# Kernel tuning notes

Hardware: AMD Instinct MI355X
Metric: run time of the kernel (lower is better)

## Reference

```python
import jax, jax.numpy as jnp
import numpy as np

HOP = jnp.array([0, 1, 4, 7, 2, 5, 8, 3, 6, 9, 11, 14, 10, 12, 15, 13, 16])
GRAPH = jnp.array([0, 1, 4, 7, 2, 5, 8, 3, 6, 9, 12, 10, 13, 15, 11, 14, 16])
D_MODEL, L, D_INNER, D_STATE, DT_RANK = 512, 17, 1024, 4, 32


def layernorm(x, w, b, eps=1e-5):
    mu = x.mean(-1, keepdims=True)
    var = ((x - mu) ** 2).mean(-1, keepdims=True)
    return (x - mu) * jax.lax.rsqrt(var + eps) * w + b


def setup_inputs() -> dict:
    key = jax.random.key(0)
    ks = jax.random.split(key, 9)
    B = 4096
    s = lambda k, shape: jax.random.normal(k, shape, jnp.float32) * 0.02
    # A_log init per mamba_ssm: log(1..d_state) repeated over d_inner
    A_log = jnp.log(jnp.broadcast_to(jnp.arange(1, D_STATE + 1, dtype=jnp.float32), (D_INNER, D_STATE)))
    return {
        "x": jax.random.normal(ks[0], (B, L, D_MODEL), jnp.float32),
        "bp_embed": s(ks[1], (1, 5, D_MODEL)),
        "ln_w": jnp.ones((D_MODEL,), jnp.float32),
        "ln_b": jnp.zeros((D_MODEL,), jnp.float32),
        "in_proj_w": s(ks[2], (2 * D_INNER, D_MODEL)),
        "conv_w": 1.0 + s(ks[3], (D_INNER,)),  # d_conv=1 depthwise conv == per-channel scale
        "conv_b": jnp.zeros((D_INNER,), jnp.float32),
        "x_proj_w": s(ks[4], (DT_RANK + 2 * D_STATE, D_INNER)),
        "dt_proj_w": s(ks[5], (D_INNER, DT_RANK)),
        "dt_proj_b": s(ks[6], (D_INNER,)) - 4.0,  # softplus-inverse-ish small dt init
        "A_log": A_log,
        "D": jnp.ones((D_INNER,), jnp.float32),
        "out_proj_w": s(ks[7], (D_MODEL, D_INNER)),
    }


def mamba(u, in_proj_w, conv_w, conv_b, x_proj_w, dt_proj_w, dt_proj_b, A_log, D, out_proj_w):
    # u: [B, L, d_model]
    xz = jnp.einsum('bld,ed->ble', u, in_proj_w)          # [B,L,2*d_inner]
    xm, z = jnp.split(xz, 2, axis=-1)
    xm = jax.nn.silu(xm * conv_w + conv_b)                 # d_conv=1 -> pointwise
    x_dbl = jnp.einsum('ble,fe->blf', xm, x_proj_w)        # [B,L,dt_rank+2*d_state]
    dt_r = x_dbl[..., :DT_RANK]
    Bm = x_dbl[..., DT_RANK:DT_RANK + D_STATE]
    Cm = x_dbl[..., DT_RANK + D_STATE:]
    dt = jax.nn.softplus(jnp.einsum('blr,er->ble', dt_r, dt_proj_w) + dt_proj_b)  # [B,L,d_inner]
    A = -jnp.exp(A_log)                                    # [d_inner,d_state]

    def step(h, inp):
        dt_t, B_t, C_t, x_t = inp                          # [B,di],[B,ds],[B,ds],[B,di]
        dA = jnp.exp(dt_t[..., None] * A)                  # [B,di,ds]
        h = dA * h + (dt_t * x_t)[..., None] * B_t[:, None, :]
        y = jnp.einsum('bes,bs->be', h, C_t)
        return h, y

    bsz = u.shape[0]
    h0 = jnp.zeros((bsz, D_INNER, D_STATE), u.dtype)
    seq = (dt.transpose(1, 0, 2), Bm.transpose(1, 0, 2), Cm.transpose(1, 0, 2), xm.transpose(1, 0, 2))
    _, ys = jax.lax.scan(step, h0, seq)                    # ys: [L,B,d_inner]
    y = ys.transpose(1, 0, 2) + xm * D
    y = y * jax.nn.silu(z)
    return jnp.einsum('ble,de->bld', y, out_proj_w)


def reference(x, bp_embed, ln_w, ln_b, in_proj_w, conv_w, conv_b, x_proj_w,
              dt_proj_w, dt_proj_b, A_log, D, out_proj_w):
    bp = bp_embed
    x_bpe = jnp.concatenate([bp[:, :3], bp[:, :3], bp[:, :3], bp[:, :1],
                             bp[:, 3:], bp[:, :1], bp[:, 3:], bp[:, 3:]], axis=1)  # [1,17,dim]
    x_ssm = x[:, HOP, :] + x_bpe
    x_ssm = layernorm(x_ssm, ln_w, ln_b)
    x_ssm = mamba(x_ssm, in_proj_w, conv_w, conv_b, x_proj_w,
                  dt_proj_w, dt_proj_b, A_log, D, out_proj_w)
    return x + x_ssm[:, GRAPH, :]
```

## Files before the change

### kernel.cpp

```cpp
#include <hip/hip_runtime.h>

typedef unsigned short u16;
typedef unsigned int   u32;
typedef __bf16 bf16_t;
typedef bf16_t bf16x8 __attribute__((ext_vector_type(8)));
typedef float  f32x4  __attribute__((ext_vector_type(4)));

#define DEV static __device__ __forceinline__

__constant__ int c_HOP[17] = {0,1,4,7,2,5,8,3,6,9,11,14,10,12,15,13,16};
__constant__ int c_BPE[17] = {0,1,2,0,1,2,0,1,2,0,3,4,0,3,4,3,4};

DEV u16 f2bf(float f){
  u32 x = __builtin_bit_cast(u32, f);
  x += 0x7fffu + ((x >> 16) & 1u);
  return (u16)(x >> 16);
}
DEV float bf2f(u32 u){ return __builtin_bit_cast(float, u << 16); }
DEV float silu_f(float v){ return v / (1.f + __expf(-v)); }
DEV float softplus_f(float s){ return (s > 20.f) ? s : log1pf(__expf(s)); }

DEV void gll16(const void* g, void* l){
  __builtin_amdgcn_global_load_lds((__attribute__((address_space(1))) void*)g,
                                   (__attribute__((address_space(3))) void*)l,
                                   16, 0, 0);
}

__global__ __launch_bounds__(256) void cvt4(
    const float* __restrict__ s0, u16* __restrict__ d0, int n0,
    const float* __restrict__ s1, u16* __restrict__ d1, int n1,
    const float* __restrict__ s2, u16* __restrict__ d2, int n2,
    const float* __restrict__ s3, u16* __restrict__ d3, int n3)
{
  int t = blockIdx.x * 256 + threadIdx.x;
  if (t < n0){ d0[t] = f2bf(s0[t]); return; }
  t -= n0; if (t < n1){ d1[t] = f2bf(s1[t]); return; }
  t -= n1; if (t < n2){ d2[t] = f2bf(s2[t]); return; }
  t -= n2; if (t < n3){ d3[t] = f2bf(s3[t]); }
}

__global__ __launch_bounds__(256) void ln_gather(
    const float* __restrict__ x, const float* __restrict__ bpe,
    const float* __restrict__ lnw, const float* __restrict__ lnb,
    u16* __restrict__ u)
{
  int tok = blockIdx.x;
  int b = tok / 17;
  int l = tok - b * 17;
  const float* xr = x   + ((size_t)b * 17 + c_HOP[l]) * 512;
  const float* br = bpe + (size_t)c_BPE[l] * 512;
  int tid = threadIdx.x;
  int d0 = tid * 2;
  float2 xv = *(const float2*)(xr + d0);
  float2 bv = *(const float2*)(br + d0);
  float v0 = xv.x + bv.x, v1 = xv.y + bv.y;

  __shared__ float red[8];
  float s = v0 + v1;
  #pragma unroll
  for (int o = 32; o; o >>= 1) s += __shfl_xor(s, o);
  if ((tid & 63) == 0) red[tid >> 6] = s;
  __syncthreads();
  float mu = (red[0] + red[1] + red[2] + red[3]) * (1.f / 512.f);
  float a0 = v0 - mu, a1 = v1 - mu;
  float q = a0 * a0 + a1 * a1;
  #pragma unroll
  for (int o = 32; o; o >>= 1) q += __shfl_xor(q, o);
  if ((tid & 63) == 0) red[4 + (tid >> 6)] = q;
  __syncthreads();
  float var = (red[4] + red[5] + red[6] + red[7]) * (1.f / 512.f);
  float rs = rsqrtf(var + 1e-5f);

  u16 o0 = f2bf(a0 * rs * lnw[d0]     + lnb[d0]);
  u16 o1 = f2bf(a1 * rs * lnw[d0 + 1] + lnb[d0 + 1]);
  u32 pack = (u32)o0 | ((u32)o1 << 16);
  *(u32*)(u + (size_t)tok * 512 + d0) = pack;
}

enum { EPI_SPLIT = 0, EPI_XDBL = 1, EPI_DT = 2, EPI_OUT = 3 };

template<int EPI>
__global__ __launch_bounds__(256) void gemm_bt(
    const u16* __restrict__ A, int lda,
    const u16* __restrict__ W, int K, int MT,
    u16* __restrict__ ob0, u16* __restrict__ ob1,
    const float* __restrict__ p0, const float* __restrict__ p1,
    const float* __restrict__ xres, float* __restrict__ fout)
{
  __shared__ u16 sA[2][128 * 32];
  __shared__ u16 sW[2][128 * 32];
  int nwg = gridDim.x;
  int cpx = nwg >> 3;
  int wg = (blockIdx.x & 7) * cpx + (blockIdx.x >> 3);
  int NT = nwg / MT;
  int nt = wg % NT, mt = wg / NT;
  int brow = mt * 128, bcol = nt * 128;
  int tid = threadIdx.x, lane = tid & 63, wid = tid >> 6;
  int wm = wid >> 1, wn = wid & 1;

  f32x4 acc[4][4] = {};

  int srow = tid >> 2;
  int sch  = tid & 3;

  const u16* gA0 = A + (size_t)(brow + srow)      * lda + (sch ^ ((srow >> 1) & 3)) * 8;
  const u16* gA1 = A + (size_t)(brow + 64 + srow) * lda + (sch ^ (((64 + srow) >> 1) & 3)) * 8;
  const u16* gW0 = W + (size_t)(bcol + srow)      * K   + (sch ^ ((srow >> 1) & 3)) * 8;
  const u16* gW1 = W + (size_t)(bcol + 64 + srow) * K   + (sch ^ (((64 + srow) >> 1) & 3)) * 8;

  auto STAGE = [&](int buf, int kt) {
    gll16(gA0 + kt, (char*)sA[buf] + tid * 16);
    gll16(gA1 + kt, (char*)sA[buf] + tid * 16 + 4096);
    gll16(gW0 + kt, (char*)sW[buf] + tid * 16);
    gll16(gW1 + kt, (char*)sW[buf] + tid * 16 + 4096);
  };

  int aoff[4], boff[4];
  #pragma unroll
  for (int mi = 0; mi < 4; mi++) {
    int r = wm * 64 + mi * 16 + (lane & 15);
    int c = (lane >> 4) ^ ((r >> 1) & 3);
    aoff[mi] = r * 64 + c * 16;
  }
  #pragma unroll
  for (int ni = 0; ni < 4; ni++) {
    int r = wn * 64 + ni * 16 + (lane & 15);
    int c = (lane >> 4) ^ ((r >> 1) & 3);
    boff[ni] = r * 64 + c * 16;
  }

  auto COMPUTE = [&](int buf) {
    bf16x8 av[4], bv[4];
    #pragma unroll
    for (int mi = 0; mi < 4; mi++)
      av[mi] = *(const bf16x8*)((const char*)sA[buf] + aoff[mi]);
    #pragma unroll
    for (int ni = 0; ni < 4; ni++)
      bv[ni] = *(const bf16x8*)((const char*)sW[buf] + boff[ni]);
    #pragma unroll
    for (int mi = 0; mi < 4; mi++)
      #pragma unroll
      for (int ni = 0; ni < 4; ni++)
        acc[mi][ni] = __builtin_amdgcn_mfma_f32_16x16x32_bf16(
            av[mi], bv[ni], acc[mi][ni], 0, 0, 0);
  };

  int nsteps = K >> 5;
  STAGE(0, 0);
  __syncthreads();
  for (int s = 0; s < nsteps; s += 2) {
    if (s + 1 < nsteps) STAGE(1, (s + 1) << 5);
    COMPUTE(0);
    __syncthreads();
    if (s + 1 < nsteps) {
      if (s + 2 < nsteps) STAGE(0, (s + 2) << 5);
      COMPUTE(1);
      __syncthreads();
    }
  }

  int r4 = (lane >> 4) * 4;
  int cl = lane & 15;
  #pragma unroll
  for (int mi = 0; mi < 4; mi++) {
    int rowb = brow + wm * 64 + mi * 16 + r4;
    #pragma unroll
    for (int ni = 0; ni < 4; ni++) {
      int col = bcol + wn * 64 + ni * 16 + cl;
      if constexpr (EPI == EPI_SPLIT) {
        bool isx = (col < 1024);
        float cw = isx ? p0[col] : 1.f;
        float cb = isx ? p1[col] : 0.f;
        u16* dst = isx ? (ob0 + col) : (ob1 + col - 1024);
        #pragma unroll
        for (int rr = 0; rr < 4; rr++)
          dst[(size_t)(rowb + rr) * 1024] = f2bf(silu_f(acc[mi][ni][rr] * cw + cb));
      } else if constexpr (EPI == EPI_XDBL) {
        if (col < 40) {
          #pragma unroll
          for (int rr = 0; rr < 4; rr++)
            ob0[(size_t)(rowb + rr) * 40 + col] = f2bf(acc[mi][ni][rr]);
        }
      } else if constexpr (EPI == EPI_DT) {
        float bb = p0[col];
        #pragma unroll
        for (int rr = 0; rr < 4; rr++)
          ob0[(size_t)(rowb + rr) * 1024 + col] = f2bf(softplus_f(acc[mi][ni][rr] + bb));
      } else {
        #pragma unroll
        for (int rr = 0; rr < 4; rr++) {
          int row = rowb + rr;
          u32 rw = (u32)row;
          u32 b = rw / 17u;
          int gl = (int)(rw - b * 17u);
          size_t oi = ((size_t)b * 17 + c_HOP[gl]) * 512 + col;
          fout[oi] = xres[oi] + acc[mi][ni][rr];
        }
      }
    }
  }
}

__global__ __launch_bounds__(128) void scan5(
    const u16* __restrict__ xm, const u16* __restrict__ zs,
    const u16* __restrict__ xdbl, u16* __restrict__ dty,
    const float* __restrict__ A_log, const float* __restrict__ Dp)
{
  int b = blockIdx.x;
  int tid = threadIdx.x;
  int e0 = tid * 8;
  const size_t base = (size_t)b * 17 * 1024;

  float4 al = *(const float4*)(A_log + (size_t)e0 * 4);
  float A0 = -__expf(al.x), A1 = -__expf(al.y);
  float A2 = -__expf(al.z), A3 = -__expf(al.w);
  float Dv[8];
  *(float4*)(Dv)     = *(const float4*)(Dp + e0);
  *(float4*)(Dv + 4) = *(const float4*)(Dp + e0 + 4);

  const u16* xmb = xm + base + e0;
  const u16* zsb = zs + base + e0;
  u16* db = dty + base + e0;
  const u16* bcb = xdbl + (size_t)b * 680 + 32;

  float h[8][4];
  #pragma unroll
  for (int c = 0; c < 8; c++)
    #pragma unroll
    for (int s = 0; s < 4; s++) h[c][s] = 0.f;

  #pragma unroll
  for (int t = 0; t < 17; t++) {
    uint4 xr = *(const uint4*)(xmb + t * 1024);
    uint4 zr = *(const uint4*)(zsb + t * 1024);
    uint4 dr = *(const uint4*)(db + t * 1024);
    uint4 bc = *(const uint4*)(bcb + t * 40);
    float B0 = bf2f(bc.x & 0xffffu), B1 = bf2f(bc.x >> 16);
    float B2 = bf2f(bc.y & 0xffffu), B3 = bf2f(bc.y >> 16);
    float C0 = bf2f(bc.z & 0xffffu), C1 = bf2f(bc.z >> 16);
    float C2 = bf2f(bc.w & 0xffffu), C3 = bf2f(bc.w >> 16);
    u32 yo[4];
    const u32* xw = (const u32*)&xr;
    const u32* zw = (const u32*)&zr;
    const u32* dw = (const u32*)&dr;
    #pragma unroll
    for (int c = 0; c < 8; c++) {
      u32 x16 = (c & 1) ? (xw[c >> 1] >> 16) : (xw[c >> 1] & 0xffffu);
      u32 z16 = (c & 1) ? (zw[c >> 1] >> 16) : (zw[c >> 1] & 0xffffu);
      u32 d16 = (c & 1) ? (dw[c >> 1] >> 16) : (dw[c >> 1] & 0xffffu);
      float xv = bf2f(x16), zv = bf2f(z16), dtv = bf2f(d16);
      float dx = dtv * xv;
      h[c][0] = __expf(dtv * A0) * h[c][0] + dx * B0;
      h[c][1] = __expf(dtv * A1) * h[c][1] + dx * B1;
      h[c][2] = __expf(dtv * A2) * h[c][2] + dx * B2;
      h[c][3] = __expf(dtv * A3) * h[c][3] + dx * B3;
      float yv = h[c][0] * C0 + h[c][1] * C1 + h[c][2] * C2 + h[c][3] * C3;
      u16 pk = f2bf((yv + xv * Dv[c]) * zv);
      if (c & 1) yo[c >> 1] |= ((u32)pk << 16);
      else       yo[c >> 1] = (u32)pk;
    }
    *(uint4*)(db + t * 1024) = *(uint4*)yo;
  }
}

extern "C" void kernel_launch(void* const* d_in, const int* in_sizes, int n_in,
                              void* d_out, int out_size, void* d_ws, size_t ws_size,
                              hipStream_t stream) {
  const float* x     = (const float*)d_in[0];
  const float* bpe   = (const float*)d_in[1];
  const float* lnw   = (const float*)d_in[2];
  const float* lnb   = (const float*)d_in[3];
  const float* w_in  = (const float*)d_in[4];
  const float* convw = (const float*)d_in[5];
  const float* convb = (const float*)d_in[6];
  const float* w_xp  = (const float*)d_in[7];
  const float* w_dt  = (const float*)d_in[8];
  const float* b_dt  = (const float*)d_in[9];
  const float* A_log = (const float*)d_in[10];
  const float* Dp    = (const float*)d_in[11];
  const float* w_out = (const float*)d_in[12];
  float* out = (float*)d_out;

  u16* ws = (u16*)d_ws;
  u16* wb_in  = ws;
  u16* wb_out = wb_in  + 1048576;
  u16* wb_xp  = wb_out + 524288;
  u16* wb_dt  = wb_xp  + 40960;
  u16* xm     = wb_dt  + 32768;
  u16* zs     = xm     + 71303168;
  u16* xdbl   = zs     + 71303168;
  u16* dty    = xdbl   + 2785280;
  u16* u      = dty;

  const int MT = 544;

  cvt4<<<6432, 256, 0, stream>>>(w_in, wb_in, 1048576, w_out, wb_out, 524288,
                                 w_xp, wb_xp, 40960, w_dt, wb_dt, 32768);

  ln_gather<<<69632, 256, 0, stream>>>(x, bpe, lnw, lnb, u);

  gemm_bt<EPI_SPLIT><<<MT * 16, 256, 0, stream>>>(
      u, 512, wb_in, 512, MT, xm, zs, convw, convb, nullptr, nullptr);

  gemm_bt<EPI_XDBL><<<MT * 1, 256, 0, stream>>>(
      xm, 1024, wb_xp, 1024, MT, xdbl, nullptr, nullptr, nullptr, nullptr, nullptr);

  gemm_bt<EPI_DT><<<MT * 8, 256, 0, stream>>>(
      xdbl, 40, wb_dt, 32, MT, dty, nullptr, b_dt, nullptr, nullptr, nullptr);

  scan5<<<4096, 128, 0, stream>>>(xm, zs, xdbl, dty, A_log, Dp);

  gemm_bt<EPI_OUT><<<MT * 4, 256, 0, stream>>>(
      dty, 1024, wb_out, 1024, MT, nullptr, nullptr, nullptr, nullptr, x, out);
}
```

Before: 985.3 us.

## Use 256x256-tile 512-thread GEMM with split-K staging for in/out projections

Adds a new gemm256 kernel with 256x256 output tiles, 8 waves and a BK=64 double buffer split into two k-halves. It interleaves async global-to-LDS loads with MFMA phases, using partial vmcnt waits and s_setprio around the MFMA bursts. The in_proj and out_proj GEMMs move to this kernel to raise data reuse per tile and reduce LDS and global traffic, while the small GEMMs keep the old kernel with a simpler loop. The trade-off is higher register and LDS pressure and fewer workgroups, e.g. only 544 blocks for out_proj.

```diff
diff --git a/kernel.cpp b/kernel.cpp
--- a/kernel.cpp
+++ b/kernel.cpp
@@ -77,15 +77,153 @@
   *(u32*)(u + (size_t)tok * 512 + d0) = pack;
 }
 
-enum { EPI_SPLIT = 0, EPI_XDBL = 1, EPI_DT = 2, EPI_OUT = 3 };
+enum { EPI_SPLIT = 0, EPI_OUT = 1, EPI_XDBL = 2, EPI_DT = 3 };
 
 template<int EPI>
-__global__ __launch_bounds__(256) void gemm_bt(
+__global__ __launch_bounds__(512, 2) void gemm256(
     const u16* __restrict__ A, int lda,
     const u16* __restrict__ W, int K, int MT,
     u16* __restrict__ ob0, u16* __restrict__ ob1,
     const float* __restrict__ p0, const float* __restrict__ p1,
     const float* __restrict__ xres, float* __restrict__ fout)
+{
+  __shared__ u16 sA[2][2][8192];
+  __shared__ u16 sB[2][2][8192];
+
+  int nwg = gridDim.x;
+  int cpx = nwg >> 3;
+  int wg = (blockIdx.x & 7) * cpx + (blockIdx.x >> 3);
+  int NT = nwg / MT;
+  int nt = wg % NT, mt = wg / NT;
+  int brow = mt * 256, bcol = nt * 256;
+  int tid = threadIdx.x, lane = tid & 63, wid = tid >> 6;
+  int wm = wid >> 2, wn = wid & 3;
+  int l15 = lane & 15, lhi = lane >> 4;
+
+  f32x4 acc[8][4] = {};
+
+  int sr0 = tid >> 2, sr1 = 128 + (tid >> 2), sch = tid & 3;
+  const u16* gA0 = A + (size_t)(brow + sr0) * lda + (sch ^ ((sr0 >> 1) & 3)) * 8;
+  const u16* gA1 = A + (size_t)(brow + sr1) * lda + (sch ^ ((sr1 >> 1) & 3)) * 8;
+  const u16* gW0 = W + (size_t)(bcol + sr0) * K   + (sch ^ ((sr0 >> 1) & 3)) * 8;
+  const u16* gW1 = W + (size_t)(bcol + sr1) * K   + (sch ^ ((sr1 >> 1) & 3)) * 8;
+
+  auto stA = [&](int buf, int kh, int koff) {
+    char* d = (char*)&sA[buf][kh][0] + tid * 16;
+    gll16(gA0 + koff, d);
+    gll16(gA1 + koff, d + 8192);
+  };
+  auto stB = [&](int buf, int kh, int koff) {
+    char* d = (char*)&sB[buf][kh][0] + tid * 16;
+    gll16(gW0 + koff, d);
+    gll16(gW1 + koff, d + 8192);
+  };
+
+  int aoff[2][4], boff[4];
+  #pragma unroll
+  for (int mh = 0; mh < 2; mh++)
+    #pragma unroll
+    for (int mi = 0; mi < 4; mi++) {
+      int r = wm * 128 + mh * 64 + mi * 16 + l15;
+      aoff[mh][mi] = r * 64 + ((lhi ^ ((r >> 1) & 3)) * 16);
+    }
+  #pragma unroll
+  for (int ni = 0; ni < 4; ni++) {
+    int r = wn * 64 + ni * 16 + l15;
+    boff[ni] = r * 64 + ((lhi ^ ((r >> 1) & 3)) * 16);
+  }
+
+  bf16x8 bvv[4];
+
+#define PHASE(buf, kh, MH, RB)                                              \
+  {                                                                         \
+    const char* la = (const char*)&sA[buf][kh][0];                          \
+    bf16x8 av0 = *(const bf16x8*)(la + aoff[MH][0]);                        \
+    bf16x8 av1 = *(const bf16x8*)(la + aoff[MH][1]);                        \
+    bf16x8 av2 = *(const bf16x8*)(la + aoff[MH][2]);                        \
+    bf16x8 av3 = *(const bf16x8*)(la + aoff[MH][3]);                        \
+    if (RB) {                                                               \
+      const char* lb = (const char*)&sB[buf][kh][0];                        \
+      bvv[0] = *(const bf16x8*)(lb + boff[0]);                              \
+      bvv[1] = *(const bf16x8*)(lb + boff[1]);                              \
+      bvv[2] = *(const bf16x8*)(lb + boff[2]);                              \
+      bvv[3] = *(const bf16x8*)(lb + boff[3]);                              \
+    }                                                                       \
+    __builtin_amdgcn_s_setprio(1);                                          \
+    _Pragma("unroll")                                                       \
+    for (int ni = 0; ni < 4; ni++) {                                        \
+      acc[(MH)*4+0][ni] = __builtin_amdgcn_mfma_f32_16x16x32_bf16(av0, bvv[ni], acc[(MH)*4+0][ni], 0,0,0); \
+      acc[(MH)*4+1][ni] = __builtin_amdgcn_mfma_f32_16x16x32_bf16(av1, bvv[ni], acc[(MH)*4+1][ni], 0,0,0); \
+      acc[(MH)*4+2][ni] = __builtin_amdgcn_mfma_f32_16x16x32_bf16(av2, bvv[ni], acc[(MH)*4+2][ni], 0,0,0); \
+      acc[(MH)*4+3][ni] = __builtin_amdgcn_mfma_f32_16x16x32_bf16(av3, bvv[ni], acc[(MH)*4+3][ni], 0,0,0); \
+    }                                                                       \
+    __builtin_amdgcn_s_setprio(0);                                          \
+  }
+
+#define WAITBAR                                                             \
+  asm volatile("s_waitcnt vmcnt(4)" ::: "memory");                          \
+  __builtin_amdgcn_s_barrier();                                             \
+  __builtin_amdgcn_sched_barrier(0);
+
+  int T = K >> 6;
+  stA(0, 0, 0); stB(0, 0, 0);
+  stA(0, 1, 32); stB(0, 1, 32);
+  WAITBAR;
+
+  for (int t = 0; t < T; ++t) {
+    int b = t & 1;
+    int nk = (t + 1) << 6;
+    bool pf = (t + 1 < T);
+    if (pf) stA(b ^ 1, 0, nk);
+    PHASE(b, 0, 0, true);
+    if (pf) stB(b ^ 1, 0, nk);
+    PHASE(b, 0, 1, false);
+    WAITBAR;
+    if (pf) stA(b ^ 1, 1, nk + 32);
+    PHASE(b, 1, 0, true);
+    if (pf) stB(b ^ 1, 1, nk + 32);
+    PHASE(b, 1, 1, false);
+    WAITBAR;
+  }
+#undef PHASE
+#undef WAITBAR
+
+  int r4 = lhi * 4;
+  #pragma unroll
+  for (int fm = 0; fm < 8; fm++) {
+    int rowb = brow + wm * 128 + fm * 16 + r4;
+    #pragma unroll
+    for (int ni = 0; ni < 4; ni++) {
+      int col = bcol + wn * 64 + ni * 16 + l15;
+      if constexpr (EPI == EPI_SPLIT) {
+        bool isx = (bcol < 1024);
+        int cidx = isx ? col : 0;
+        float cw = isx ? p0[cidx] : 1.f;
+        float cb = isx ? p1[cidx] : 0.f;
+        u16* dst = isx ? (ob0 + col) : (ob1 + col - 1024);
+        #pragma unroll
+        for (int rr = 0; rr < 4; rr++)
+          dst[(size_t)(rowb + rr) * 1024] = f2bf(silu_f(acc[fm][ni][rr] * cw + cb));
+      } else {
+        #pragma unroll
+        for (int rr = 0; rr < 4; rr++) {
+          int row = rowb + rr;
+          u32 rw = (u32)row;
+          u32 b = rw / 17u;
+          int gl = (int)(rw - b * 17u);
+          size_t oi = ((size_t)b * 17 + c_HOP[gl]) * 512 + col;
+          fout[oi] = xres[oi] + acc[fm][ni][rr];
+        }
+      }
+    }
+  }
+}
+
+template<int EPI>
+__global__ __launch_bounds__(256) void gemm_bt(
+    const u16* __restrict__ A, int lda,
+    const u16* __restrict__ W, int K, int MT,
+    u16* __restrict__ ob0, const float* __restrict__ p0)
 {
   __shared__ u16 sA[2][128 * 32];
   __shared__ u16 sW[2][128 * 32];
@@ -119,14 +257,12 @@
   #pragma unroll
   for (int mi = 0; mi < 4; mi++) {
     int r = wm * 64 + mi * 16 + (lane & 15);
-    int c = (lane >> 4) ^ ((r >> 1) & 3);
-    aoff[mi] = r * 64 + c * 16;
+    aoff[mi] = r * 64 + (((lane >> 4) ^ ((r >> 1) & 3)) * 16);
   }
   #pragma unroll
   for (int ni = 0; ni < 4; ni++) {
     int r = wn * 64 + ni * 16 + (lane & 15);
-    int c = (lane >> 4) ^ ((r >> 1) & 3);
-    boff[ni] = r * 64 + c * 16;
+    boff[ni] = r * 64 + (((lane >> 4) ^ ((r >> 1) & 3)) * 16);
   }
 
   auto COMPUTE = [&](int buf) {
@@ -148,16 +284,14 @@
   int nsteps = K >> 5;
   STAGE(0, 0);
   __syncthreads();
-  for (int s = 0; s < nsteps; s += 2) {
-    if (s + 1 < nsteps) STAGE(1, (s + 1) << 5);
-    COMPUTE(0);
+  int cur = 0;
+  for (int s = 1; s < nsteps; ++s) {
+    STAGE(cur ^ 1, s << 5);
+    COMPUTE(cur);
     __syncthreads();
-    if (s + 1 < nsteps) {
-      if (s + 2 < nsteps) STAGE(0, (s + 2) << 5);
-      COMPUTE(1);
-      __syncthreads();
-    }
-  }
+    cur ^= 1;
+  }
+  COMPUTE(cur);
 
   int r4 = (lane >> 4) * 4;
   int cl = lane & 15;
@@ -167,35 +301,17 @@
     #pragma unroll
     for (int ni = 0; ni < 4; ni++) {
       int col = bcol + wn * 64 + ni * 16 + cl;
-      if constexpr (EPI == EPI_SPLIT) {
-        bool isx = (col < 1024);
-        float cw = isx ? p0[col] : 1.f;
-        float cb = isx ? p1[col] : 0.f;
-        u16* dst = isx ? (ob0 + col) : (ob1 + col - 1024);
-        #pragma unroll
-        for (int rr = 0; rr < 4; rr++)
-          dst[(size_t)(rowb + rr) * 1024] = f2bf(silu_f(acc[mi][ni][rr] * cw + cb));
-      } else if constexpr (EPI == EPI_XDBL) {
+      if constexpr (EPI == EPI_XDBL) {
         if (col < 40) {
           #pragma unroll
           for (int rr = 0; rr < 4; rr++)
             ob0[(size_t)(rowb + rr) * 40 + col] = f2bf(acc[mi][ni][rr]);
         }
-      } else if constexpr (EPI == EPI_DT) {
+      } else {
         float bb = p0[col];
         #pragma unroll
         for (int rr = 0; rr < 4; rr++)
           ob0[(size_t)(rowb + rr) * 1024 + col] = f2bf(softplus_f(acc[mi][ni][rr] + bb));
-      } else {
-        #pragma unroll
-        for (int rr = 0; rr < 4; rr++) {
-          int row = rowb + rr;
-          u32 rw = (u32)row;
-          u32 b = rw / 17u;
-          int gl = (int)(rw - b * 17u);
-          size_t oi = ((size_t)b * 17 + c_HOP[gl]) * 512 + col;
-          fout[oi] = xres[oi] + acc[mi][ni][rr];
-        }
       }
     }
   }
@@ -292,24 +408,25 @@
   u16* dty    = xdbl   + 2785280;
   u16* u      = dty;
 
-  const int MT = 544;
+  const int MT2 = 272;
+  const int MT1 = 544;
 
   cvt4<<<6432, 256, 0, stream>>>(w_in, wb_in, 1048576, w_out, wb_out, 524288,
                                  w_xp, wb_xp, 40960, w_dt, wb_dt, 32768);
 
   ln_gather<<<69632, 256, 0, stream>>>(x, bpe, lnw, lnb, u);
 
-  gemm_bt<EPI_SPLIT><<<MT * 16, 256, 0, stream>>>(
-      u, 512, wb_in, 512, MT, xm, zs, convw, convb, nullptr, nullptr);
-
-  gemm_bt<EPI_XDBL><<<MT * 1, 256, 0, stream>>>(
-      xm, 1024, wb_xp, 1024, MT, xdbl, nullptr, nullptr, nullptr, nullptr, nullptr);
-
-  gemm_bt<EPI_DT><<<MT * 8, 256, 0, stream>>>(
-      xdbl, 40, wb_dt, 32, MT, dty, nullptr, b_dt, nullptr, nullptr, nullptr);
+  gemm256<EPI_SPLIT><<<MT2 * 8, 512, 0, stream>>>(
+      u, 512, wb_in, 512, MT2, xm, zs, convw, convb, nullptr, nullptr);
+
+  gemm_bt<EPI_XDBL><<<MT1 * 1, 256, 0, stream>>>(
+      xm, 1024, wb_xp, 1024, MT1, xdbl, nullptr);
+
+  gemm_bt<EPI_DT><<<MT1 * 8, 256, 0, stream>>>(
+      xdbl, 40, wb_dt, 32, MT1, dty, b_dt);
 
   scan5<<<4096, 128, 0, stream>>>(xm, zs, xdbl, dty, A_log, Dp);
 
-  gemm_bt<EPI_OUT><<<MT * 4, 256, 0, stream>>>(
-      dty, 1024, wb_out, 1024, MT, nullptr, nullptr, nullptr, nullptr, x, out);
-}
+  gemm256<EPI_OUT><<<MT2 * 2, 512, 0, stream>>>(
+      dty, 1024, wb_out, 1024, MT2, nullptr, nullptr, nullptr, nullptr, x, out);
+}
```

After: 894.6 us. 9.2% less time.
